# Performance work log

Hardware: AMD Instinct MI355X
Metric: run time of the kernel (lower is better)

The kernel has to match this reference:

```python
import jax, jax.numpy as jnp
import numpy as np

MARGIN = 0.3


def setup_inputs() -> dict:
    key = jax.random.key(0)
    k1, k2 = jax.random.split(key)
    embeddings = jax.random.normal(k1, (4096, 128), dtype=jnp.float32)
    labels = jax.random.randint(k2, (4096,), 0, 256, dtype=jnp.int64)
    return {"embeddings": embeddings, "labels": labels}


def reference(embeddings, labels):
    # L2-normalize rows (same as F.normalize(p=2, dim=1), eps=1e-12)
    norm = jnp.maximum(jnp.linalg.norm(embeddings, axis=1, keepdims=True), 1e-12)
    e = embeddings / norm
    # cosine distance matrix [N, N]
    dist = 1.0 - e @ e.T

    same = labels[None, :] == labels[:, None]          # [N, N]
    n = labels.shape[0]
    eye = jnp.eye(n, dtype=bool)
    pos_mask = same & ~eye                             # positives excl. self
    neg_mask = ~same

    # dist in [0, 2]; finite sentinels keep max/min well-defined per row
    hardest_pos = jnp.max(jnp.where(pos_mask, dist, -1.0), axis=1)
    hardest_neg = jnp.min(jnp.where(neg_mask, dist, 3.0), axis=1)

    valid = jnp.any(pos_mask, axis=1) & jnp.any(neg_mask, axis=1)
    per_row = jax.nn.relu(hardest_pos - hardest_neg + MARGIN)
    loss_sum = jnp.sum(jnp.where(valid, per_row, 0.0))
    count = jnp.sum(valid)
    return loss_sum / jnp.maximum(count, 1).astype(loss_sum.dtype)
```

## Files before the change

### kernel.cpp

```cpp
#include <hip/hip_runtime.h>
#include <stdint.h>

typedef __bf16 bf16x8 __attribute__((ext_vector_type(8)));
typedef float f32x4 __attribute__((ext_vector_type(4)));

#define N_ROWS 4096
#define KD 128
#define BM 64
#define NCHUNK 32
#define CHUNK 128
#define NBLOCKS (64 * NCHUNK)
#define FIN_BLOCKS 64

__device__ __forceinline__ unsigned short f32_to_bf16_rne(float f) {
    union { float f; uint32_t u; } v; v.f = f;
    uint32_t u = v.u;
    return (unsigned short)((u + 0x7FFFu + ((u >> 16) & 1u)) >> 16);
}

__device__ __forceinline__ int swz(int row, int c) { return row * 16 + (c ^ (row & 15)); }
__device__ __forceinline__ int swzL(int L) { return (L & ~15) | ((L & 15) ^ ((L >> 4) & 15)); }

__global__ __launch_bounds__(256) void normalize_kernel(const float* __restrict__ E,
                                                        unsigned short* __restrict__ out,
                                                        unsigned* __restrict__ ctrl) {
    if (blockIdx.x == 0 && threadIdx.x < 3) ctrl[threadIdx.x] = 0u;
    const int wave = threadIdx.x >> 6;
    const int lane = threadIdx.x & 63;
    const int row = blockIdx.x * 4 + wave;
    const float2 v = *(const float2*)&E[row * KD + lane * 2];
    float s = v.x * v.x + v.y * v.y;
#pragma unroll
    for (int m = 1; m < 64; m <<= 1) s += __shfl_xor(s, m, 64);
    float inv = 0.0f;
    if (s > 0.0f) {
        inv = rsqrtf(s);
        inv = inv * (1.5f - 0.5f * s * inv * inv);
    }
    const unsigned short a = f32_to_bf16_rne(v.x * inv);
    const unsigned short b = f32_to_bf16_rne(v.y * inv);
    ((uint32_t*)out)[row * (KD / 2) + lane] = ((uint32_t)b << 16) | a;
}

__global__ __launch_bounds__(256) void gram_kernel(const unsigned short* __restrict__ Ebits,
                                                   const int* __restrict__ labels,
                                                   float2* __restrict__ partials) {
    __shared__ uint4 Bs4[CHUNK * (KD / 8)];
    __shared__ int ljs[CHUNK];

    const int tid = threadIdx.x;
    const int itile = blockIdx.x & 63;
    const int chunk = blockIdx.x >> 6;
    const int ibase = itile * BM;
    const int cbase = chunk * CHUNK;

    const int wave = tid >> 6, lane = tid & 63;
    const int quad = lane >> 4, l15 = lane & 15;
    const int igb = ibase + wave * 16 + quad * 4;

    {
        const uint4* src = (const uint4*)(Ebits + (size_t)cbase * KD);
#pragma unroll
        for (int it = 0; it < 8; ++it) {
            const int L = it * 256 + tid;
            Bs4[swzL(L)] = src[L];
        }
    }
    if (tid < CHUNK) ljs[tid] = labels[cbase + tid];

    bf16x8 afrag[4];
    {
        const uint4* asrc = (const uint4*)Ebits;
        const int arow = ibase + wave * 16 + l15;
#pragma unroll
        for (int s = 0; s < 4; ++s) afrag[s] = *(const bf16x8*)&asrc[arow * 16 + s * 4 + quad];
    }
    int li_lab[4];
#pragma unroll
    for (int r = 0; r < 4; ++r) li_lab[r] = labels[igb + r];

    __syncthreads();

    float minpos[4] = {2.0f, 2.0f, 2.0f, 2.0f};
    float maxneg[4] = {-2.0f, -2.0f, -2.0f, -2.0f};

#pragma unroll
    for (int t = 0; t < 8; ++t) {
        f32x4 acc = {0.f, 0.f, 0.f, 0.f};
#pragma unroll
        for (int s = 0; s < 4; ++s) {
            const bf16x8 bfrag = *(const bf16x8*)&Bs4[swz(t * 16 + l15, s * 4 + quad)];
            acc = __builtin_amdgcn_mfma_f32_16x16x32_bf16(afrag[s], bfrag, acc, 0, 0, 0);
        }
        const int jg = cbase + t * 16 + l15;
        const int lj = ljs[t * 16 + l15];
#pragma unroll
        for (int r = 0; r < 4; ++r) {
            const float d = acc[r];
            const bool same = (lj == li_lab[r]);
            const float dp = (same && (igb + r != jg)) ? d : 2.0f;
            const float dn = same ? -2.0f : d;
            minpos[r] = fminf(minpos[r], dp);
            maxneg[r] = fmaxf(maxneg[r], dn);
        }
    }

#pragma unroll
    for (int m = 1; m < 16; m <<= 1) {
#pragma unroll
        for (int r = 0; r < 4; ++r) {
            minpos[r] = fminf(minpos[r], __shfl_xor(minpos[r], m, 64));
            maxneg[r] = fmaxf(maxneg[r], __shfl_xor(maxneg[r], m, 64));
        }
    }
    if (l15 == 0) {
#pragma unroll
        for (int r = 0; r < 4; ++r)
            partials[(igb + r) * NCHUNK + chunk] = make_float2(minpos[r], maxneg[r]);
    }
}

__global__ __launch_bounds__(256) void finalize_kernel(const float2* __restrict__ partials,
                                                       float* __restrict__ gsum,
                                                       unsigned* __restrict__ gcnt,
                                                       unsigned* __restrict__ ticket,
                                                       float* __restrict__ out) {
    __shared__ float ssum[4];
    __shared__ int scnt[4];
    __shared__ unsigned s_old;

    const int tid = threadIdx.x;
    const int sub = tid & 3;
    const int row = blockIdx.x * 64 + (tid >> 2);

    const float4* p4 = (const float4*)&partials[row * NCHUNK];
    float mp = 2.f, mn = -2.f;
#pragma unroll
    for (int k = 0; k < 4; ++k) {
        const float4 v = p4[sub * 4 + k];
        mp = fminf(mp, fminf(v.x, v.z));
        mn = fmaxf(mn, fmaxf(v.y, v.w));
    }
    mp = fminf(mp, __shfl_xor(mp, 1, 64)); mp = fminf(mp, __shfl_xor(mp, 2, 64));
    mn = fmaxf(mn, __shfl_xor(mn, 1, 64)); mn = fmaxf(mn, __shfl_xor(mn, 2, 64));

    float sum = 0.f; int cnt = 0;
    if (sub == 0 && mp < 1.5f && mn > -1.5f) {
        sum = fmaxf(0.f, mn - mp + 0.3f);
        cnt = 1;
    }
#pragma unroll
    for (int m = 1; m < 64; m <<= 1) {
        sum += __shfl_xor(sum, m, 64);
        cnt += __shfl_xor(cnt, m, 64);
    }
    const int wave = tid >> 6, lane = tid & 63;
    if (lane == 0) { ssum[wave] = sum; scnt[wave] = cnt; }
    __syncthreads();
    if (tid == 0) {
        atomicAdd(gsum, ssum[0] + ssum[1] + ssum[2] + ssum[3]);
        atomicAdd(gcnt, (unsigned)(scnt[0] + scnt[1] + scnt[2] + scnt[3]));
    }
    __syncthreads();
    if (tid == 0) s_old = atomicAdd(ticket, 1u);
    __syncthreads();
    if (s_old == (unsigned)(FIN_BLOCKS - 1) && tid == 0) {
        const float S = __hip_atomic_load(gsum, __ATOMIC_RELAXED, __HIP_MEMORY_SCOPE_AGENT);
        const unsigned C = __hip_atomic_load(gcnt, __ATOMIC_RELAXED, __HIP_MEMORY_SCOPE_AGENT);
        out[0] = S / (float)(C > 0u ? C : 1u);
    }
}

extern "C" void kernel_launch(void* const* d_in, const int* in_sizes, int n_in,
                              void* d_out, int out_size, void* d_ws, size_t ws_size,
                              hipStream_t stream) {
    const float* E = (const float*)d_in[0];
    const int* labels = (const int*)d_in[1];

    unsigned short* ebits = (unsigned short*)d_ws;
    float2* partials = (float2*)((char*)d_ws + (size_t)N_ROWS * KD * 2);
    unsigned* ctrl = (unsigned*)(partials + N_ROWS * NCHUNK);
    float* gsum = (float*)&ctrl[0];
    unsigned* gcnt = &ctrl[1];
    unsigned* ticket = &ctrl[2];
    float* out = (float*)d_out;

    normalize_kernel<<<N_ROWS / 4, 256, 0, stream>>>(E, ebits, ctrl);
    gram_kernel<<<NBLOCKS, 256, 0, stream>>>(ebits, labels, partials);
    finalize_kernel<<<FIN_BLOCKS, 256, 0, stream>>>(partials, gsum, gcnt, ticket, out);
}
```

Before: 72.56 us.

## Fuse finalize into gram kernel via order-preserving atomic min/max and ticket

Drops the partials buffer and the separate finalize kernel. Each gram block now folds its per-row hardest-positive and hardest-negative values into global per-row slots, using atomicMin/atomicMax on an order-preserving unsigned encoding of the float. The last block to finish, chosen by a ticket counter, reduces all 4096 rows and writes the loss. This saves one kernel launch and the partials round trip, at the cost of 8192 atomics per block group, contention on shared row slots, and a serial tail where one block scans every row.

```diff
diff --git a/kernel.cpp b/kernel.cpp
--- a/kernel.cpp
+++ b/kernel.cpp
@@ -10,7 +10,19 @@
 #define NCHUNK 32
 #define CHUNK 128
 #define NBLOCKS (64 * NCHUNK)
-#define FIN_BLOCKS 64
+
+#define ENC_POS2 0xC0000000u
+#define ENC_NEG2 0x3FFFFFFFu
+
+__device__ __forceinline__ unsigned enc_f32(float f) {
+    union { float f; unsigned u; } v; v.f = f;
+    return (v.u & 0x80000000u) ? ~v.u : (v.u | 0x80000000u);
+}
+__device__ __forceinline__ float dec_f32(unsigned e) {
+    union { float f; unsigned u; } v;
+    v.u = (e & 0x80000000u) ? (e ^ 0x80000000u) : ~e;
+    return v.f;
+}
 
 __device__ __forceinline__ unsigned short f32_to_bf16_rne(float f) {
     union { float f; uint32_t u; } v; v.f = f;
@@ -23,11 +35,19 @@
 
 __global__ __launch_bounds__(256) void normalize_kernel(const float* __restrict__ E,
                                                         unsigned short* __restrict__ out,
-                                                        unsigned* __restrict__ ctrl) {
-    if (blockIdx.x == 0 && threadIdx.x < 3) ctrl[threadIdx.x] = 0u;
+                                                        unsigned* __restrict__ hp,
+                                                        unsigned* __restrict__ hn,
+                                                        unsigned* __restrict__ ticket) {
+    const int r0 = blockIdx.x * 4;
+    if (threadIdx.x < 4) {
+        hp[r0 + threadIdx.x] = ENC_POS2;
+        hn[r0 + threadIdx.x] = ENC_NEG2;
+    }
+    if (blockIdx.x == 0 && threadIdx.x == 0) *ticket = 0u;
+
     const int wave = threadIdx.x >> 6;
     const int lane = threadIdx.x & 63;
-    const int row = blockIdx.x * 4 + wave;
+    const int row = r0 + wave;
     const float2 v = *(const float2*)&E[row * KD + lane * 2];
     float s = v.x * v.x + v.y * v.y;
 #pragma unroll
@@ -44,9 +64,15 @@
 
 __global__ __launch_bounds__(256) void gram_kernel(const unsigned short* __restrict__ Ebits,
                                                    const int* __restrict__ labels,
-                                                   float2* __restrict__ partials) {
+                                                   unsigned* __restrict__ hp,
+                                                   unsigned* __restrict__ hn,
+                                                   unsigned* __restrict__ ticket,
+                                                   float* __restrict__ out) {
     __shared__ uint4 Bs4[CHUNK * (KD / 8)];
     __shared__ int ljs[CHUNK];
+    __shared__ unsigned s_old;
+    __shared__ float ssum[4];
+    __shared__ int scnt[4];
 
     const int tid = threadIdx.x;
     const int itile = blockIdx.x & 63;
@@ -113,61 +139,44 @@
             maxneg[r] = fmaxf(maxneg[r], __shfl_xor(maxneg[r], m, 64));
         }
     }
+
     if (l15 == 0) {
 #pragma unroll
-        for (int r = 0; r < 4; ++r)
-            partials[(igb + r) * NCHUNK + chunk] = make_float2(minpos[r], maxneg[r]);
+        for (int r = 0; r < 4; ++r) {
+            atomicMin(&hp[igb + r], enc_f32(minpos[r]));
+            atomicMax(&hn[igb + r], enc_f32(maxneg[r]));
+        }
     }
-}
 
-__global__ __launch_bounds__(256) void finalize_kernel(const float2* __restrict__ partials,
-                                                       float* __restrict__ gsum,
-                                                       unsigned* __restrict__ gcnt,
-                                                       unsigned* __restrict__ ticket,
-                                                       float* __restrict__ out) {
-    __shared__ float ssum[4];
-    __shared__ int scnt[4];
-    __shared__ unsigned s_old;
-
-    const int tid = threadIdx.x;
-    const int sub = tid & 3;
-    const int row = blockIdx.x * 64 + (tid >> 2);
-
-    const float4* p4 = (const float4*)&partials[row * NCHUNK];
-    float mp = 2.f, mn = -2.f;
-#pragma unroll
-    for (int k = 0; k < 4; ++k) {
-        const float4 v = p4[sub * 4 + k];
-        mp = fminf(mp, fminf(v.x, v.z));
-        mn = fmaxf(mn, fmaxf(v.y, v.w));
-    }
-    mp = fminf(mp, __shfl_xor(mp, 1, 64)); mp = fminf(mp, __shfl_xor(mp, 2, 64));
-    mn = fmaxf(mn, __shfl_xor(mn, 1, 64)); mn = fmaxf(mn, __shfl_xor(mn, 2, 64));
+    __syncthreads();
+    if (tid == 0) s_old = atomicAdd(ticket, 1u);
+    __syncthreads();
+    if (s_old != (unsigned)(NBLOCKS - 1)) return;
 
     float sum = 0.f; int cnt = 0;
-    if (sub == 0 && mp < 1.5f && mn > -1.5f) {
-        sum = fmaxf(0.f, mn - mp + 0.3f);
-        cnt = 1;
+#pragma unroll
+    for (int k = 0; k < 16; ++k) {
+        const int row = k * 256 + tid;
+        const unsigned ep = __hip_atomic_load(&hp[row], __ATOMIC_RELAXED, __HIP_MEMORY_SCOPE_AGENT);
+        const unsigned en = __hip_atomic_load(&hn[row], __ATOMIC_RELAXED, __HIP_MEMORY_SCOPE_AGENT);
+        const float mp = dec_f32(ep);
+        const float mn = dec_f32(en);
+        if (mp < 1.5f && mn > -1.5f) {
+            sum += fmaxf(0.f, mn - mp + 0.3f);
+            ++cnt;
+        }
     }
 #pragma unroll
     for (int m = 1; m < 64; m <<= 1) {
         sum += __shfl_xor(sum, m, 64);
         cnt += __shfl_xor(cnt, m, 64);
     }
-    const int wave = tid >> 6, lane = tid & 63;
     if (lane == 0) { ssum[wave] = sum; scnt[wave] = cnt; }
     __syncthreads();
     if (tid == 0) {
-        atomicAdd(gsum, ssum[0] + ssum[1] + ssum[2] + ssum[3]);
-        atomicAdd(gcnt, (unsigned)(scnt[0] + scnt[1] + scnt[2] + scnt[3]));
-    }
-    __syncthreads();
-    if (tid == 0) s_old = atomicAdd(ticket, 1u);
-    __syncthreads();
-    if (s_old == (unsigned)(FIN_BLOCKS - 1) && tid == 0) {
-        const float S = __hip_atomic_load(gsum, __ATOMIC_RELAXED, __HIP_MEMORY_SCOPE_AGENT);
-        const unsigned C = __hip_atomic_load(gcnt, __ATOMIC_RELAXED, __HIP_MEMORY_SCOPE_AGENT);
-        out[0] = S / (float)(C > 0u ? C : 1u);
+        const float S = ssum[0] + ssum[1] + ssum[2] + ssum[3];
+        const int C = scnt[0] + scnt[1] + scnt[2] + scnt[3];
+        out[0] = S / (float)(C > 0 ? C : 1);
     }
 }
 
@@ -178,14 +187,11 @@
     const int* labels = (const int*)d_in[1];
 
     unsigned short* ebits = (unsigned short*)d_ws;
-    float2* partials = (float2*)((char*)d_ws + (size_t)N_ROWS * KD * 2);
-    unsigned* ctrl = (unsigned*)(partials + N_ROWS * NCHUNK);
-    float* gsum = (float*)&ctrl[0];
-    unsigned* gcnt = &ctrl[1];
-    unsigned* ticket = &ctrl[2];
+    unsigned* hp = (unsigned*)((char*)d_ws + (size_t)N_ROWS * KD * 2);
+    unsigned* hn = hp + N_ROWS;
+    unsigned* ticket = hn + N_ROWS;
     float* out = (float*)d_out;
 
-    normalize_kernel<<<N_ROWS / 4, 256, 0, stream>>>(E, ebits, ctrl);
-    gram_kernel<<<NBLOCKS, 256, 0, stream>>>(ebits, labels, partials);
-    finalize_kernel<<<FIN_BLOCKS, 256, 0, stream>>>(partials, gsum, gcnt, ticket, out);
+    normalize_kernel<<<N_ROWS / 4, 256, 0, stream>>>(E, ebits, hp, hn, ticket);
+    gram_kernel<<<NBLOCKS, 256, 0, stream>>>(ebits, labels, hp, hn, ticket, out);
 }
```

New measurement: 86.99 us. 1.2x slower.

## Double gram row tile per block and load B chunk via direct global-to-LDS

Applied to the files above, without the earlier changes.

Each wave now computes two 16-row MFMA tiles against the same shared B fragment, doubling the row tile to 128 and halving the block count, so each B chunk staged in LDS is reused across twice as many rows. The B chunk is also loaded with global_load_lds, which writes straight into LDS without passing through registers, and the source addresses are pre-swizzled so the existing swizzled reads still apply. This cuts redundant B loads and register staging. The cost is more registers per wave and fewer blocks to fill the CUs, plus a launch_bounds occupancy hint.

```diff
diff --git a/kernel.cpp b/kernel.cpp
--- a/kernel.cpp
+++ b/kernel.cpp
@@ -6,10 +6,10 @@
 
 #define N_ROWS 4096
 #define KD 128
-#define BM 64
+#define BM 128
 #define NCHUNK 32
 #define CHUNK 128
-#define NBLOCKS (64 * NCHUNK)
+#define NBLOCKS (32 * NCHUNK)
 #define FIN_BLOCKS 64
 
 __device__ __forceinline__ unsigned short f32_to_bf16_rne(float f) {
@@ -42,81 +42,103 @@
     ((uint32_t*)out)[row * (KD / 2) + lane] = ((uint32_t)b << 16) | a;
 }
 
-__global__ __launch_bounds__(256) void gram_kernel(const unsigned short* __restrict__ Ebits,
-                                                   const int* __restrict__ labels,
-                                                   float2* __restrict__ partials) {
+__global__ __launch_bounds__(256, 4) void gram_kernel(const unsigned short* __restrict__ Ebits,
+                                                      const int* __restrict__ labels,
+                                                      float2* __restrict__ partials) {
     __shared__ uint4 Bs4[CHUNK * (KD / 8)];
     __shared__ int ljs[CHUNK];
 
     const int tid = threadIdx.x;
-    const int itile = blockIdx.x & 63;
-    const int chunk = blockIdx.x >> 6;
+    const int itile = blockIdx.x & 31;
+    const int chunk = blockIdx.x >> 5;
     const int ibase = itile * BM;
     const int cbase = chunk * CHUNK;
 
     const int wave = tid >> 6, lane = tid & 63;
     const int quad = lane >> 4, l15 = lane & 15;
-    const int igb = ibase + wave * 16 + quad * 4;
 
     {
         const uint4* src = (const uint4*)(Ebits + (size_t)cbase * KD);
 #pragma unroll
         for (int it = 0; it < 8; ++it) {
-            const int L = it * 256 + tid;
-            Bs4[swzL(L)] = src[L];
+            const int Ld = it * 256 + wave * 64 + lane;
+            const int Ls = swzL(Ld);
+            __builtin_amdgcn_global_load_lds(
+                (const __attribute__((address_space(1))) void*)&src[Ls],
+                (__attribute__((address_space(3))) void*)&Bs4[it * 256 + wave * 64],
+                16, 0, 0);
         }
     }
     if (tid < CHUNK) ljs[tid] = labels[cbase + tid];
 
-    bf16x8 afrag[4];
+    bf16x8 afrag[2][4];
     {
         const uint4* asrc = (const uint4*)Ebits;
-        const int arow = ibase + wave * 16 + l15;
-#pragma unroll
-        for (int s = 0; s < 4; ++s) afrag[s] = *(const bf16x8*)&asrc[arow * 16 + s * 4 + quad];
-    }
-    int li_lab[4];
-#pragma unroll
-    for (int r = 0; r < 4; ++r) li_lab[r] = labels[igb + r];
-
-    __syncthreads();
-
-    float minpos[4] = {2.0f, 2.0f, 2.0f, 2.0f};
-    float maxneg[4] = {-2.0f, -2.0f, -2.0f, -2.0f};
+#pragma unroll
+        for (int mb = 0; mb < 2; ++mb) {
+            const int arow = ibase + wave * 32 + mb * 16 + l15;
+#pragma unroll
+            for (int s = 0; s < 4; ++s)
+                afrag[mb][s] = *(const bf16x8*)&asrc[arow * 16 + s * 4 + quad];
+        }
+    }
+    int li_lab[2][4];
+#pragma unroll
+    for (int mb = 0; mb < 2; ++mb)
+#pragma unroll
+        for (int r = 0; r < 4; ++r)
+            li_lab[mb][r] = labels[ibase + wave * 32 + mb * 16 + quad * 4 + r];
+
+    __syncthreads();
+
+    float minpos[2][4] = {{2.f, 2.f, 2.f, 2.f}, {2.f, 2.f, 2.f, 2.f}};
+    float maxneg[2][4] = {{-2.f, -2.f, -2.f, -2.f}, {-2.f, -2.f, -2.f, -2.f}};
 
 #pragma unroll
     for (int t = 0; t < 8; ++t) {
-        f32x4 acc = {0.f, 0.f, 0.f, 0.f};
+        f32x4 acc0 = {0.f, 0.f, 0.f, 0.f};
+        f32x4 acc1 = {0.f, 0.f, 0.f, 0.f};
 #pragma unroll
         for (int s = 0; s < 4; ++s) {
             const bf16x8 bfrag = *(const bf16x8*)&Bs4[swz(t * 16 + l15, s * 4 + quad)];
-            acc = __builtin_amdgcn_mfma_f32_16x16x32_bf16(afrag[s], bfrag, acc, 0, 0, 0);
+            acc0 = __builtin_amdgcn_mfma_f32_16x16x32_bf16(afrag[0][s], bfrag, acc0, 0, 0, 0);
+            acc1 = __builtin_amdgcn_mfma_f32_16x16x32_bf16(afrag[1][s], bfrag, acc1, 0, 0, 0);
         }
         const int jg = cbase + t * 16 + l15;
         const int lj = ljs[t * 16 + l15];
 #pragma unroll
-        for (int r = 0; r < 4; ++r) {
-            const float d = acc[r];
-            const bool same = (lj == li_lab[r]);
-            const float dp = (same && (igb + r != jg)) ? d : 2.0f;
-            const float dn = same ? -2.0f : d;
-            minpos[r] = fminf(minpos[r], dp);
-            maxneg[r] = fmaxf(maxneg[r], dn);
+        for (int mb = 0; mb < 2; ++mb) {
+            const int ig0 = ibase + wave * 32 + mb * 16 + quad * 4;
+#pragma unroll
+            for (int r = 0; r < 4; ++r) {
+                const float d = (mb == 0) ? acc0[r] : acc1[r];
+                const bool same = (lj == li_lab[mb][r]);
+                const float dp = (same && (ig0 + r != jg)) ? d : 2.0f;
+                const float dn = same ? -2.0f : d;
+                minpos[mb][r] = fminf(minpos[mb][r], dp);
+                maxneg[mb][r] = fmaxf(maxneg[mb][r], dn);
+            }
         }
     }
 
 #pragma unroll
     for (int m = 1; m < 16; m <<= 1) {
 #pragma unroll
-        for (int r = 0; r < 4; ++r) {
-            minpos[r] = fminf(minpos[r], __shfl_xor(minpos[r], m, 64));
-            maxneg[r] = fmaxf(maxneg[r], __shfl_xor(maxneg[r], m, 64));
-        }
+        for (int mb = 0; mb < 2; ++mb)
+#pragma unroll
+            for (int r = 0; r < 4; ++r) {
+                minpos[mb][r] = fminf(minpos[mb][r], __shfl_xor(minpos[mb][r], m, 64));
+                maxneg[mb][r] = fmaxf(maxneg[mb][r], __shfl_xor(maxneg[mb][r], m, 64));
+            }
     }
     if (l15 == 0) {
 #pragma unroll
-        for (int r = 0; r < 4; ++r)
-            partials[(igb + r) * NCHUNK + chunk] = make_float2(minpos[r], maxneg[r]);
+        for (int mb = 0; mb < 2; ++mb) {
+            const int ig0 = ibase + wave * 32 + mb * 16 + quad * 4;
+#pragma unroll
+            for (int r = 0; r < 4; ++r)
+                partials[(ig0 + r) * NCHUNK + chunk] = make_float2(minpos[mb][r], maxneg[mb][r]);
+        }
     }
 }
 
```

Result: no change. 72.27 us (-0.4%).
